# Kernel optimization log

Hardware: AMD Instinct MI355X
Metric: run time of the kernel (lower is better)

## Reference

```python
import jax, jax.numpy as jnp
import numpy as np

T, B, M, A, H = 2048, 128, 32, 32, 64
G = M + A + H  # gate input features (mass_in_gates=True)


def _l1norm(a):
    # F.normalize(p=1, dim=-1): a / max(sum|a|, 1e-12); a is sigmoid output (>0)
    return a / jnp.maximum(jnp.sum(jnp.abs(a), axis=-1, keepdims=True), 1e-12)


def setup_inputs() -> dict:
    key = jax.random.key(0)
    ks = jax.random.split(key, 5)
    ortho = jax.nn.initializers.orthogonal()
    return {
        "x_m": jax.random.uniform(ks[0], (T, B, M), dtype=jnp.float32),
        "x_a": jax.random.normal(ks[1], (T, B, A), dtype=jnp.float32),
        "Wi": ortho(ks[2], (G, M * H), jnp.float32),  # input gate
        "bi": jnp.zeros((M * H,), jnp.float32),
        "Wr": ortho(ks[3], (G, H * H), jnp.float32),  # redistribution
        "br": jnp.zeros((H * H,), jnp.float32),
        "Wo": ortho(ks[4], (G, H), jnp.float32),      # output gate
        "bo": jnp.zeros((H,), jnp.float32),
    }


def reference(x_m, x_a, Wi, bi, Wr, br, Wo, bo):
    def step(c, xs):
        xt_m, xt_a = xs  # [B,M], [B,A]
        # NOTE: torch c.norm(1) (no dim) = scalar L1 norm of whole [B,H] tensor
        cn = c / (jnp.sum(jnp.abs(c)) + 1e-5)
        feat = jnp.concatenate([xt_m, xt_a, cn], axis=-1)  # [B,G]
        i = _l1norm(jax.nn.sigmoid(feat @ Wi + bi).reshape(-1, M, H))  # [B,M,H]
        r = _l1norm(jax.nn.sigmoid(feat @ Wr + br).reshape(-1, H, H))  # [B,H,H]
        o = jax.nn.sigmoid(feat @ Wo + bo)                              # [B,H]
        m_new = jnp.einsum('bm,bmh->bh', xt_m, i) + jnp.einsum('bk,bkh->bh', c, r)
        m_out = o * m_new
        c_new = (1.0 - o) * m_new  # subtract_outgoing_mass=True
        return c_new, (m_out, c_new)

    c0 = jnp.zeros((x_m.shape[1], H), x_m.dtype)
    _, (m_out, c) = jax.lax.scan(step, c0, (x_m, x_a))
    return m_out, c
```

## Files before the change

kernel.cpp:

```cpp
#include <hip/hip_runtime.h>
#include <hip/hip_fp16.h>


#define TT 2048
#define NBS 8
#define NUS 7
#define NWG 56

typedef _Float16 f16;
typedef _Float16 f16x8 __attribute__((ext_vector_type(8)));
typedef float f32x4 __attribute__((ext_vector_type(4)));

#define LD_RLX(p)   __hip_atomic_load((p), __ATOMIC_RELAXED, __HIP_MEMORY_SCOPE_AGENT)
#define ST_RLX(p,v) __hip_atomic_store((p), (v), __ATOMIC_RELAXED, __HIP_MEMORY_SCOPE_AGENT)

static __device__ __forceinline__ unsigned packf16(float v, unsigned tag) {
  f16 h = (f16)v;
  unsigned short s;
  __builtin_memcpy(&s, &h, 2);
  return ((unsigned)s << 16) | (tag & 0xffffu);
}
static __device__ __forceinline__ float unpackf16(unsigned u) {
  unsigned short s = (unsigned short)(u >> 16);
  f16 h;
  __builtin_memcpy(&h, &s, 2);
  return (float)h;
}
static __device__ __forceinline__ float f16bits(unsigned short s) {
  f16 h;
  __builtin_memcpy(&h, &s, 2);
  return (float)h;
}
static __device__ __forceinline__ unsigned short f16of(float v) {
  f16 h = (f16)v;
  unsigned short s;
  __builtin_memcpy(&s, &h, 2);
  return s;
}

#define OFF_WH   0u
#define SZ_WH    (97u * 8192u * 2u)
#define OFF_SLAB ((OFF_WH + SZ_WH + 255u) & ~255u)
#define SZ_SLAB  (2u * NBS * NUS * 1024u * 4u)
#define OFF_NS   (OFF_SLAB + SZ_SLAB)
#define SZ_NS    (2u * NBS * 4u)
#define ZERO_OFF OFF_SLAB
#define ZERO_LEN (SZ_SLAB + SZ_NS)

__global__ void prep_kernel(const float* __restrict__ Wi, const float* __restrict__ Wr,
                            const float* __restrict__ Wo, f16* __restrict__ Wh) {
  int idx = blockIdx.x * 256 + threadIdx.x;
  if (idx >= 97 * 8192) return;
  int g = idx & 127, h = (idx >> 7) & 63, r = idx >> 13;
  float v;
  if (r < 32)      v = Wi[g * 2048 + r * 64 + h];
  else if (r < 96) v = Wr[g * 4096 + (r - 32) * 64 + h];
  else             v = Wo[g * 64 + h];
  Wh[idx] = (f16)v;
}

__launch_bounds__(512)
__attribute__((amdgpu_waves_per_eu(2, 2)))
__global__ void mclstm_kernel(const float* __restrict__ xm, const float* __restrict__ xa,
                              const float* __restrict__ bi, const float* __restrict__ br,
                              const float* __restrict__ bo, const f16* __restrict__ Wh,
                              unsigned* __restrict__ slab, unsigned* __restrict__ nslab,
                              float* __restrict__ out) {
  const int j = blockIdx.x, tid = threadIdx.x;
  const int us = j % NUS, bs = j / NUS;
  const int w = tid >> 6, l = tid & 63, lr = l & 15, lk = l >> 4;
  const bool isO = (us == 6);
  const bool isIWG = (us < 2);

  __shared__ unsigned short craw[16][88];
  __shared__ float pslab[8][1024];
  __shared__ float nredL[8];
  __shared__ float invS;

  for (int i = tid; i < 16 * 88; i += 512) (&craw[0][0])[i] = 0;
  if (tid == 0) invS = 0.f;

  f16x8 Bf[2][4][4];
  float bu[2][4];
#pragma unroll
  for (int un = 0; un < 2; ++un) {
    int u = isO ? 96 : us * 16 + 2 * w + un;
#pragma unroll
    for (int ht = 0; ht < 4; ++ht) {
      int col = ht * 16 + lr;
      bu[un][ht] = (u < 32) ? bi[u * 64 + col]
                 : (u < 96) ? br[(u - 32) * 64 + col] : bo[col];
#pragma unroll
      for (int kk = 0; kk < 4; ++kk)
        Bf[un][ht][kk] = *(const f16x8*)(Wh + (size_t)u * 8192 + col * 128 + kk * 32 + lk * 8);
    }
  }

  const size_t xoff = (size_t)(bs * 16 + lr) * 32 + lk * 8;
  f32x4 xA0 = *(const f32x4*)(xm + xoff), xA1 = *(const f32x4*)(xm + xoff + 4);
  f32x4 xB0 = *(const f32x4*)(xa + xoff), xB1 = *(const f32x4*)(xa + xoff + 4);
  __syncthreads();

  for (int t = 0; t <= TT; ++t) {
    float xw[2][4];
    f32x4 aX[2][4];
    if (t < TT) {
      if (isIWG) {
        const float* xmtp = xm + (size_t)t * 4096;
#pragma unroll
        for (int rr = 0; rr < 4; ++rr) {
          const size_t ro = (size_t)(bs * 16 + lk * 4 + rr) * 32 + us * 16 + 2 * w;
          xw[0][rr] = xmtp[ro];
          xw[1][rr] = xmtp[ro + 1];
        }
      }
      f16x8 A0, A1;
#pragma unroll
      for (int i = 0; i < 4; ++i) {
        A0[i] = (f16)xA0[i]; A0[4 + i] = (f16)xA1[i];
        A1[i] = (f16)xB0[i]; A1[4 + i] = (f16)xB1[i];
      }
      if (t + 1 < TT) {
        const float* bx = xm + (size_t)(t + 1) * 4096 + xoff;
        const float* ba = xa + (size_t)(t + 1) * 4096 + xoff;
        xA0 = *(const f32x4*)bx; xA1 = *(const f32x4*)(bx + 4);
        xB0 = *(const f32x4*)ba; xB1 = *(const f32x4*)(ba + 4);
      }
      if (!isO || w == 0) {
#pragma unroll
        for (int un = 0; un < 2; ++un)
#pragma unroll
          for (int ht = 0; ht < 4; ++ht) {
            f32x4 a = (f32x4){0.f, 0.f, 0.f, 0.f};
            a = __builtin_amdgcn_mfma_f32_16x16x32_f16(A0, Bf[un][ht][0], a, 0, 0, 0);
            a = __builtin_amdgcn_mfma_f32_16x16x32_f16(A1, Bf[un][ht][1], a, 0, 0, 0);
            aX[un][ht] = a;
          }
      }
    }

    if (t > 0) {
      const unsigned want = (unsigned)t & 0xffffu;
      const unsigned* base = slab + ((size_t)(t & 1) * NBS + bs) * (NUS * 1024);
      {
        const unsigned* gp = base + l * 1024 + 128 * w;
        for (;;) {
          unsigned v = (l < NUS) ? LD_RLX(gp) : want;
          if (__all((int)((v & 0xffffu) == want))) break;
          __builtin_amdgcn_s_sleep(1);
        }
      }
      const int e0 = 2 * tid;
      unsigned pv[14];
      for (;;) {
#pragma unroll
        for (int c = 0; c < 7; ++c) {
          pv[c] = LD_RLX(base + c * 1024 + e0);
          pv[7 + c] = LD_RLX(base + c * 1024 + e0 + 1);
        }
        unsigned m = 0;
#pragma unroll
        for (int c = 0; c < 14; ++c) m |= (pv[c] ^ want) & 0xffffu;
        if (m == 0) break;
        __builtin_amdgcn_s_sleep(1);
      }
      float mn0 = 0.f, mn1 = 0.f;
#pragma unroll
      for (int c = 0; c < 6; ++c) {
        mn0 += unpackf16(pv[c]);
        mn1 += unpackf16(pv[7 + c]);
      }
      const float ov0 = unpackf16(pv[6]), ov1 = unpackf16(pv[13]);
      const float cn0 = (1.0f - ov0) * mn0, cn1 = (1.0f - ov1) * mn1;
      const unsigned short h0 = f16of(cn0), h1 = f16of(cn1);
      const int b = e0 >> 6, h = e0 & 63;
      craw[b][h] = h0;
      craw[b][h + 1] = h1;
      if (isO) {
        float ns = fabsf(f16bits(h0)) + fabsf(f16bits(h1));
        ns += __shfl_xor(ns, 1, 64);
        ns += __shfl_xor(ns, 2, 64);
        ns += __shfl_xor(ns, 4, 64);
        ns += __shfl_xor(ns, 8, 64);
        ns += __shfl_xor(ns, 16, 64);
        ns += __shfl_xor(ns, 32, 64);
        if (l == 0) nredL[w] = ns;
        __syncthreads();
        if (tid == 0) {
          float nsum = 0.f;
#pragma unroll
          for (int p = 0; p < 8; ++p) nsum += nredL[p];
          ST_RLX(nslab + (t & 1) * NBS + bs, packf16(nsum, (unsigned)t));
        }
        const int bg = bs * 16 + b;
        out[(size_t)(t - 1) * 8192 + bg * 64 + h] = ov0 * mn0;
        out[(size_t)(t - 1) * 8192 + bg * 64 + h + 1] = ov1 * mn1;
        out[(size_t)(TT + t - 1) * 8192 + bg * 64 + h] = cn0;
        out[(size_t)(TT + t - 1) * 8192 + bg * 64 + h + 1] = cn1;
      }
    }
    if (t == TT) break;
    __syncthreads();

    f16x8 A2, A3;
    {
      const unsigned short* cr = &craw[lr][0];
#pragma unroll
      for (int i = 0; i < 8; ++i) A2[i] = *(const f16*)&cr[lk * 8 + i];
#pragma unroll
      for (int i = 0; i < 8; ++i) A3[i] = *(const f16*)&cr[32 + lk * 8 + i];
    }
    f32x4 aC[2][4];
    if (!isO || w == 0) {
#pragma unroll
      for (int un = 0; un < 2; ++un)
#pragma unroll
        for (int ht = 0; ht < 4; ++ht) {
          f32x4 c = (f32x4){0.f, 0.f, 0.f, 0.f};
          c = __builtin_amdgcn_mfma_f32_16x16x32_f16(A2, Bf[un][ht][2], c, 0, 0, 0);
          c = __builtin_amdgcn_mfma_f32_16x16x32_f16(A3, Bf[un][ht][3], c, 0, 0, 0);
          aC[un][ht] = c;
        }
    }

    if (t > 0 && w == 0) {
      const unsigned want = (unsigned)t & 0xffffu;
      const unsigned* nsb = nslab + (t & 1) * NBS;
      unsigned v;
      for (;;) {
        v = (l < NBS) ? LD_RLX(nsb + l) : want;
        if (__all((int)((v & 0xffffu) == want))) break;
        __builtin_amdgcn_s_sleep(1);
      }
      float ns = (l < NBS) ? unpackf16(v) : 0.f;
      ns += __shfl_xor(ns, 1, 64);
      ns += __shfl_xor(ns, 2, 64);
      ns += __shfl_xor(ns, 4, 64);
      if (l == 0) invS = __builtin_amdgcn_rcpf(ns + 1e-5f);
    }
    __syncthreads();
    const float inv = invS;

    if (!isO) {
      float contrib[4][4];
#pragma unroll
      for (int ht = 0; ht < 4; ++ht)
#pragma unroll
        for (int rr = 0; rr < 4; ++rr) contrib[ht][rr] = 0.f;
#pragma unroll
      for (int un = 0; un < 2; ++un) {
        const int kidx = us * 16 + 2 * w + un - 32;
#pragma unroll
        for (int rr = 0; rr < 4; ++rr) {
          const int b = lk * 4 + rr;
          float s4[4], sum = 0.f;
#pragma unroll
          for (int ht = 0; ht < 4; ++ht) {
            float z = aX[un][ht][rr] + inv * aC[un][ht][rr] + bu[un][ht];
            float sg = __builtin_amdgcn_rcpf(1.0f + __expf(-z));
            s4[ht] = sg;
            sum += sg;
          }
          float r4 = sum;
          r4 += __shfl_xor(r4, 1, 64);
          r4 += __shfl_xor(r4, 2, 64);
          r4 += __shfl_xor(r4, 4, 64);
          r4 += __shfl_xor(r4, 8, 64);
          float wr = isIWG ? xw[un][rr] : f16bits(craw[b][kidx]);
          float sc = wr * __builtin_amdgcn_rcpf(fmaxf(r4, 1e-12f));
#pragma unroll
          for (int ht = 0; ht < 4; ++ht) contrib[ht][rr] += s4[ht] * sc;
        }
      }
#pragma unroll
      for (int ht = 0; ht < 4; ++ht)
#pragma unroll
        for (int rr = 0; rr < 4; ++rr)
          pslab[w][(lk * 4 + rr) * 64 + ht * 16 + lr] = contrib[ht][rr];
    } else if (w == 0) {
#pragma unroll
      for (int ht = 0; ht < 4; ++ht)
#pragma unroll
        for (int rr = 0; rr < 4; ++rr) {
          float z = aX[0][ht][rr] + inv * aC[0][ht][rr] + bu[0][ht];
          pslab[0][(lk * 4 + rr) * 64 + ht * 16 + lr] =
              __builtin_amdgcn_rcpf(1.0f + __expf(-z));
        }
    }
    __syncthreads();

    {
      const int e0 = 2 * tid;
      float v0, v1;
      if (!isO) {
        v0 = 0.f; v1 = 0.f;
#pragma unroll
        for (int p = 0; p < 8; ++p) {
          float2 pv2 = *(const float2*)&pslab[p][e0];
          v0 += pv2.x;
          v1 += pv2.y;
        }
      } else {
        float2 pv2 = *(const float2*)&pslab[0][e0];
        v0 = pv2.x;
        v1 = pv2.y;
      }
      const unsigned tg = (unsigned)(t + 1);
      unsigned* dst = slab + ((size_t)((t + 1) & 1) * NBS + bs) * (NUS * 1024) + us * 1024;
      ST_RLX(dst + e0, packf16(v0, tg));
      ST_RLX(dst + e0 + 1, packf16(v1, tg));
    }
  }
}

extern "C" void kernel_launch(void* const* d_in, const int* in_sizes, int n_in,
                              void* d_out, int out_size, void* d_ws, size_t ws_size,
                              hipStream_t stream) {
  (void)in_sizes; (void)n_in; (void)out_size; (void)ws_size;
  const float* xm = (const float*)d_in[0];
  const float* xa = (const float*)d_in[1];
  const float* Wi = (const float*)d_in[2];
  const float* bi = (const float*)d_in[3];
  const float* Wr = (const float*)d_in[4];
  const float* br = (const float*)d_in[5];
  const float* Wo = (const float*)d_in[6];
  const float* bo = (const float*)d_in[7];

  char* ws = (char*)d_ws;
  f16* Wh         = (f16*)(ws + OFF_WH);
  unsigned* slab  = (unsigned*)(ws + OFF_SLAB);
  unsigned* nslab = (unsigned*)(ws + OFF_NS);

  hipMemsetAsync(ws + ZERO_OFF, 0, ZERO_LEN, stream);
  prep_kernel<<<(97 * 8192 + 255) / 256, 256, 0, stream>>>(Wi, Wr, Wo, Wh);
  mclstm_kernel<<<NWG, 512, 0, stream>>>(xm, xa, bi, br, bo, Wh, slab, nslab,
                                         (float*)d_out);
}
```

Baseline: 17.72 ms.

## Distribute norm reduction and output writes across all workgroups, drop extra barrier

Every workgroup now computes its own partial L1 norm of the cell state and publishes it to a per-(batch-slice, unit-slice) slot. All waves read the 56 partial norms directly with a ballot-based tag check, so the shared-memory broadcast of invS and one __syncthreads per step go away. Output stores are spread across workgroups by thread ownership and moved to the end of the step, off the critical path. Other changes: the sleep in the slab spin loop is removed, the two slab stores are packed into one 64-bit atomic, and the waves_per_eu attribute is dropped. The cost is more global polling traffic, since every wave spins on 56 flags instead of 8.

After: 24.21 ms. 1.37x slower.

```diff
diff --git a/kernel.cpp b/kernel.cpp
--- a/kernel.cpp
+++ b/kernel.cpp
@@ -43,7 +43,7 @@
 #define OFF_SLAB ((OFF_WH + SZ_WH + 255u) & ~255u)
 #define SZ_SLAB  (2u * NBS * NUS * 1024u * 4u)
 #define OFF_NS   (OFF_SLAB + SZ_SLAB)
-#define SZ_NS    (2u * NBS * 4u)
+#define SZ_NS    (2u * 64u * 4u)
 #define ZERO_OFF OFF_SLAB
 #define ZERO_LEN (SZ_SLAB + SZ_NS)
 
@@ -60,7 +60,6 @@
 }
 
 __launch_bounds__(512)
-__attribute__((amdgpu_waves_per_eu(2, 2)))
 __global__ void mclstm_kernel(const float* __restrict__ xm, const float* __restrict__ xa,
                               const float* __restrict__ bi, const float* __restrict__ br,
                               const float* __restrict__ bo, const f16* __restrict__ Wh,
@@ -71,14 +70,13 @@
   const int w = tid >> 6, l = tid & 63, lr = l & 15, lk = l >> 4;
   const bool isO = (us == 6);
   const bool isIWG = (us < 2);
+  const bool ownOut = ((tid * 7) >> 9) == us;
 
   __shared__ unsigned short craw[16][88];
   __shared__ float pslab[8][1024];
   __shared__ float nredL[8];
-  __shared__ float invS;
 
   for (int i = tid; i < 16 * 88; i += 512) (&craw[0][0])[i] = 0;
-  if (tid == 0) invS = 0.f;
 
   f16x8 Bf[2][4][4];
   float bu[2][4];
@@ -100,6 +98,8 @@
   f32x4 xA0 = *(const f32x4*)(xm + xoff), xA1 = *(const f32x4*)(xm + xoff + 4);
   f32x4 xB0 = *(const f32x4*)(xa + xoff), xB1 = *(const f32x4*)(xa + xoff + 4);
   __syncthreads();
+
+  float ov0 = 0.f, ov1 = 0.f, mn0 = 0.f, mn1 = 0.f, cn0 = 0.f, cn1 = 0.f;
 
   for (int t = 0; t <= TT; ++t) {
     float xw[2][4];
@@ -162,45 +162,49 @@
 #pragma unroll
         for (int c = 0; c < 14; ++c) m |= (pv[c] ^ want) & 0xffffu;
         if (m == 0) break;
-        __builtin_amdgcn_s_sleep(1);
-      }
-      float mn0 = 0.f, mn1 = 0.f;
+      }
+      mn0 = 0.f; mn1 = 0.f;
 #pragma unroll
       for (int c = 0; c < 6; ++c) {
         mn0 += unpackf16(pv[c]);
         mn1 += unpackf16(pv[7 + c]);
       }
-      const float ov0 = unpackf16(pv[6]), ov1 = unpackf16(pv[13]);
-      const float cn0 = (1.0f - ov0) * mn0, cn1 = (1.0f - ov1) * mn1;
+      ov0 = unpackf16(pv[6]);
+      ov1 = unpackf16(pv[13]);
+      cn0 = (1.0f - ov0) * mn0;
+      cn1 = (1.0f - ov1) * mn1;
       const unsigned short h0 = f16of(cn0), h1 = f16of(cn1);
       const int b = e0 >> 6, h = e0 & 63;
       craw[b][h] = h0;
       craw[b][h + 1] = h1;
-      if (isO) {
-        float ns = fabsf(f16bits(h0)) + fabsf(f16bits(h1));
-        ns += __shfl_xor(ns, 1, 64);
-        ns += __shfl_xor(ns, 2, 64);
-        ns += __shfl_xor(ns, 4, 64);
-        ns += __shfl_xor(ns, 8, 64);
-        ns += __shfl_xor(ns, 16, 64);
-        ns += __shfl_xor(ns, 32, 64);
-        if (l == 0) nredL[w] = ns;
-        __syncthreads();
-        if (tid == 0) {
-          float nsum = 0.f;
-#pragma unroll
-          for (int p = 0; p < 8; ++p) nsum += nredL[p];
-          ST_RLX(nslab + (t & 1) * NBS + bs, packf16(nsum, (unsigned)t));
-        }
+      float ns = fabsf(f16bits(h0)) + fabsf(f16bits(h1));
+      ns += __shfl_xor(ns, 1, 64);
+      ns += __shfl_xor(ns, 2, 64);
+      ns += __shfl_xor(ns, 4, 64);
+      ns += __shfl_xor(ns, 8, 64);
+      ns += __shfl_xor(ns, 16, 64);
+      ns += __shfl_xor(ns, 32, 64);
+      if (l == 0) nredL[w] = ns;
+    }
+    if (t == TT) {
+      if (ownOut) {
+        const int e0 = 2 * tid, b = e0 >> 6, h = e0 & 63;
         const int bg = bs * 16 + b;
         out[(size_t)(t - 1) * 8192 + bg * 64 + h] = ov0 * mn0;
         out[(size_t)(t - 1) * 8192 + bg * 64 + h + 1] = ov1 * mn1;
         out[(size_t)(TT + t - 1) * 8192 + bg * 64 + h] = cn0;
         out[(size_t)(TT + t - 1) * 8192 + bg * 64 + h + 1] = cn1;
       }
-    }
-    if (t == TT) break;
+      break;
+    }
     __syncthreads();
+
+    if (t > 0 && tid == 0) {
+      float nsum = 0.f;
+#pragma unroll
+      for (int p = 0; p < 8; ++p) nsum += nredL[p];
+      ST_RLX(nslab + (t & 1) * 64 + bs * 8 + us, packf16(nsum, (unsigned)t));
+    }
 
     f16x8 A2, A3;
     {
@@ -223,23 +227,34 @@
         }
     }
 
-    if (t > 0 && w == 0) {
+    float inv = 0.f;
+    if (t > 0) {
       const unsigned want = (unsigned)t & 0xffffu;
-      const unsigned* nsb = nslab + (t & 1) * NBS;
-      unsigned v;
+      const unsigned* nsb = nslab + (t & 1) * 64;
+      unsigned v = 0;
+      unsigned long long bal;
       for (;;) {
-        v = (l < NBS) ? LD_RLX(nsb + l) : want;
-        if (__all((int)((v & 0xffffu) == want))) break;
+        bool mt = false;
+        if ((l & 7) < NUS) {
+          v = LD_RLX(nsb + l);
+          mt = ((v ^ want) & 0xffffu) == 0;
+        }
+        bal = __ballot((int)mt);
+        bool ok = true;
+#pragma unroll
+        for (int g = 0; g < 8; ++g) ok &= ((bal >> (8 * g)) & 0x7Full) != 0ull;
+        if (ok) break;
         __builtin_amdgcn_s_sleep(1);
       }
-      float ns = (l < NBS) ? unpackf16(v) : 0.f;
-      ns += __shfl_xor(ns, 1, 64);
-      ns += __shfl_xor(ns, 2, 64);
-      ns += __shfl_xor(ns, 4, 64);
-      if (l == 0) invS = __builtin_amdgcn_rcpf(ns + 1e-5f);
-    }
-    __syncthreads();
-    const float inv = invS;
+      float nm = 0.f;
+#pragma unroll
+      for (int g = 0; g < 8; ++g) {
+        int lg = 8 * g + __builtin_ctzll((bal >> (8 * g)) & 0x7Full);
+        unsigned vg = __shfl(v, lg, 64);
+        nm += unpackf16(vg);
+      }
+      inv = __builtin_amdgcn_rcpf(nm + 1e-5f);
+    }
 
     if (!isO) {
       float contrib[4][4];
@@ -307,8 +322,19 @@
       }
       const unsigned tg = (unsigned)(t + 1);
       unsigned* dst = slab + ((size_t)((t + 1) & 1) * NBS + bs) * (NUS * 1024) + us * 1024;
-      ST_RLX(dst + e0, packf16(v0, tg));
-      ST_RLX(dst + e0 + 1, packf16(v1, tg));
+      unsigned long long q =
+          ((unsigned long long)packf16(v1, tg) << 32) | (unsigned long long)packf16(v0, tg);
+      __hip_atomic_store((unsigned long long*)(dst + e0), q, __ATOMIC_RELAXED,
+                         __HIP_MEMORY_SCOPE_AGENT);
+    }
+
+    if (t > 0 && ownOut) {
+      const int e0 = 2 * tid, b = e0 >> 6, h = e0 & 63;
+      const int bg = bs * 16 + b;
+      out[(size_t)(t - 1) * 8192 + bg * 64 + h] = ov0 * mn0;
+      out[(size_t)(t - 1) * 8192 + bg * 64 + h + 1] = ov1 * mn1;
+      out[(size_t)(TT + t - 1) * 8192 + bg * 64 + h] = cn0;
+      out[(size_t)(TT + t - 1) * 8192 + bg * 64 + h + 1] = cn1;
     }
   }
 }
```
